# Performance work log

Measured on AMD Instinct MI355X. Metric: run time of the kernel, lower is better.

The kernel has to match this reference:

```python
import jax, jax.numpy as jnp
import numpy as np

N_QUBITS = 8
D_K = 64
B, S = 8, 1024


def _single_qubit_states(xang, theta):
    # xang: [B,S,n] values in [-1,1] (post-tanh); theta: [n,3] Rot params (phi, theta, omega)
    # state = RZ(omega) @ RY(th) @ RZ(phi) @ RY(pi*xang) |0>
    a = xang * jnp.pi
    c = jnp.cos(a * 0.5)          # [B,S,n]
    s = jnp.sin(a * 0.5)
    phi, th, om = theta[:, 0], theta[:, 1], theta[:, 2]   # each [n]
    ct = jnp.cos(th * 0.5)
    st = jnp.sin(th * 0.5)
    e_mpo = jnp.exp(-0.5j * (phi + om))   # e^{-i(phi+omega)/2}
    e_pmo = jnp.exp(0.5j * (phi - om))    # e^{+i(phi-omega)/2}
    amp0 = e_mpo * ct * c - e_pmo * st * s
    amp1 = jnp.conj(e_pmo) * st * c + jnp.conj(e_mpo) * ct * s
    return jnp.stack([amp0, amp1], axis=-1)   # [B,S,n,2] complex64


def setup_inputs() -> dict:
    key = jax.random.key(0)
    k1, k2, k3, k4 = jax.random.split(key, 4)
    x = jax.random.normal(k1, (B, S, D_K), dtype=jnp.float32)
    theta_q = jax.random.normal(k2, (N_QUBITS, 3), dtype=jnp.float32) * 0.1
    theta_k = jax.random.normal(k3, (N_QUBITS, 3), dtype=jnp.float32) * 0.1
    W_v = jax.random.normal(k4, (D_K, D_K), dtype=jnp.float32) / np.sqrt(D_K)
    b_v = jnp.zeros((D_K,), dtype=jnp.float32)
    return {"x": x, "theta_q": theta_q, "theta_k": theta_k, "W_v": W_v, "b_v": b_v}


def reference(x, theta_q, theta_k, W_v, b_v):
    n = theta_q.shape[0]
    xn = jnp.tanh(x[..., :n])                 # [B,S,n]
    qs = _single_qubit_states(xn, theta_q)    # [B,S,n,2]
    ks = _single_qubit_states(xn, theta_k)    # [B,S,n,2]
    # per-qubit overlap <q_i | k_j> for every (b, s, t) pair
    ov = jnp.einsum('bsnc,btnc->bstn', jnp.conj(qs), ks)  # [B,S,S,n] complex
    mag2 = jnp.real(ov) ** 2 + jnp.imag(ov) ** 2
    core = jnp.prod(mag2, axis=-1)            # |<psi_q|psi_k>|^2 = swap-test <Z>
    scores = (core + 1.0) * 0.5               # [B,S,S]
    attn = jax.nn.softmax(scores, axis=-1)
    values = x @ W_v.T + b_v                  # [B,S,D]
    out = jnp.einsum('bst,btd->bsd', attn, values)
    return out, attn
```

## Files before the change

kernel.cpp:

```cpp
#include <hip/hip_runtime.h>
#include <hip/hip_fp16.h>
#include <math.h>

#define NQ 8
#define DK 64
#define NB 8
#define NS 1024
#define RB 8
#define EPITCH 1032

typedef _Float16 h2v __attribute__((ext_vector_type(2)));

__device__ __forceinline__ float fdot2h(unsigned qu, unsigned ku, float acc) {
#if defined(__has_builtin) && __has_builtin(__builtin_amdgcn_fdot2)
    union { unsigned u; h2v h; } a, b;
    a.u = qu; b.u = ku;
    return __builtin_amdgcn_fdot2(a.h, b.h, acc, false);
#else
    __half2 qh = *(__half2*)&qu, kh = *(__half2*)&ku;
    float2 qf = __half22float2(qh), kf = __half22float2(kh);
    return fmaf(qf.x, kf.x, fmaf(qf.y, kf.y, acc));
#endif
}

__device__ __forceinline__ void qk_density(float s, float c,
                                           const float* t6,
                                           float& d0, float& d1, float& ur, float& ui) {
    float ct = t6[0], st = t6[1], cmpo = t6[2], smpo = t6[3], cpmo = t6[4], spmo = t6[5];
    float a = ct * c, b2 = st * s, cc = st * c, d2 = ct * s;
    float a0re =  cmpo * a - cpmo * b2;
    float a0im = -smpo * a - spmo * b2;
    float a1re =  cpmo * cc + cmpo * d2;
    float a1im = -spmo * cc + smpo * d2;
    d0 = fmaf(a0re, a0re, a0im * a0im);
    d1 = fmaf(a1re, a1re, a1im * a1im);
    ur = fmaf(a1re, a0re, a1im * a0im);
    ui = fmaf(a1im, a0re, -a1re * a0im);
}

__device__ __forceinline__ void theta_table(const float* __restrict__ thp, int n, float* t6) {
    float phi = thp[n * 3 + 0], th = thp[n * 3 + 1], om = thp[n * 3 + 2];
    float st, ct; __sincosf(0.5f * th, &st, &ct);
    float smpo, cmpo; __sincosf(0.5f * (phi + om), &smpo, &cmpo);
    float spmo, cpmo; __sincosf(0.5f * (phi - om), &spmo, &cpmo);
    t6[0] = ct; t6[1] = st; t6[2] = cmpo; t6[3] = smpo; t6[4] = cpmo; t6[5] = spmo;
}

__device__ __forceinline__ void tanh_sincos(float xin, float& s, float& c) {
    float ex = __expf(2.0f * xin);
    float xn = 1.0f - 2.0f / (ex + 1.0f);
    __sincosf(xn * 1.57079632679489662f, &s, &c);
}

__global__ __launch_bounds__(256) void prep_kernel(
    const float* __restrict__ x,
    const float* __restrict__ theta_k,
    const float* __restrict__ Wv,
    const float* __restrict__ bv,
    __half* __restrict__ kdh,
    __half* __restrict__ v2) {
    int bid = blockIdx.x;
    int tid = threadIdx.x;
    if (bid < 1024) {
        int gp = bid * 4 + (tid >> 6);
        int d = tid & 63;
        int t0 = gp * 2;
        const float4* x0 = (const float4*)(x + (size_t)t0 * DK);
        const float4* x1 = (const float4*)(x + (size_t)(t0 + 1) * DK);
        const float4* wr = (const float4*)(Wv + (size_t)d * DK);
        float p0 = bv[d], p1 = bv[d], q0 = 0.f, q1 = 0.f;
#pragma unroll
        for (int j = 0; j < DK / 4; ++j) {
            float4 wv = wr[j];
            float4 a = x0[j], b = x1[j];
            p0 = fmaf(a.x, wv.x, p0); q0 = fmaf(a.y, wv.y, q0);
            p0 = fmaf(a.z, wv.z, p0); q0 = fmaf(a.w, wv.w, q0);
            p1 = fmaf(b.x, wv.x, p1); q1 = fmaf(b.y, wv.y, q1);
            p1 = fmaf(b.z, wv.z, p1); q1 = fmaf(b.w, wv.w, q1);
        }
        int b = t0 >> 10, pi = (t0 & 1023) >> 1;
        __half2 hv = __floats2half2_rn(p0 + q0, p1 + q1);
        *(__half2*)&v2[((size_t)(b * 512 + pi) * 64 + d) * 2] = hv;
    } else {
        __shared__ float tk[NQ][6];
        if (tid < NQ) theta_table(theta_k, tid, tk[tid]);
        __syncthreads();

        int gid = (bid - 1024) * 256 + tid;
        int tok = gid >> 3;
        int n = gid & 7;
        float s, c;
        tanh_sincos(x[(size_t)tok * DK + n], s, c);
        float d0, d1, ur, ui;
        qk_density(s, c, tk[n], d0, d1, ur, ui);
        __half2* kp = (__half2*)(kdh + (size_t)tok * 32 + n * 4);
        kp[0] = __floats2half2_rn(d0, d1);
        kp[1] = __floats2half2_rn(2.f * ur, 2.f * ui);
    }
}

__global__ __launch_bounds__(256, 4) void attn_kernel(
    const float* __restrict__ x,
    const float* __restrict__ theta_q,
    const __half* __restrict__ kdh,
    const __half* __restrict__ v2,
    float* __restrict__ out, float* __restrict__ attn) {
    __shared__ __align__(16) unsigned char smem[RB * EPITCH * 2];
    __half (*e16)[EPITCH] = (__half(*)[EPITCH])smem;
    float* red = (float*)smem;
    __shared__ unsigned q16[RB][16];
    __shared__ float tq[NQ][6];
    __shared__ float red_lds[4][RB];
    __shared__ float inv_lds[RB];

    int tid = threadIdx.x;
    int gr0 = blockIdx.x * RB;
    int b = gr0 >> 10;
    int w = tid >> 6, lane = tid & 63;

    if (tid < NQ) theta_table(theta_q, tid, tq[tid]);
    __syncthreads();
    if (tid < RB * NQ) {
        int r = tid >> 3, n = tid & 7;
        float s, c;
        tanh_sincos(x[(size_t)(gr0 + r) * DK + n], s, c);
        float d0, d1, ur, ui;
        qk_density(s, c, tq[n], d0, d1, ur, ui);
        __half2 h0 = __floats2half2_rn(d0, d1);
        __half2 h1 = __floats2half2_rn(ur, ui);
        q16[r][2 * n + 0] = *(unsigned*)&h0;
        q16[r][2 * n + 1] = *(unsigned*)&h1;
    }

    const __half* kfb = kdh + (size_t)b * NS * 32;
    int t0 = w * 256;
    uint4 kv[4][4];
#pragma unroll
    for (int j = 0; j < 4; ++j) {
        const uint4* kp = (const uint4*)(kfb + (size_t)(t0 + j * 64 + lane) * 32);
        kv[j][0] = kp[0]; kv[j][1] = kp[1]; kv[j][2] = kp[2]; kv[j][3] = kp[3];
    }
    __syncthreads();

    float sums[RB];
#pragma unroll
    for (int r = 0; r < RB; ++r) sums[r] = 0.f;

#pragma unroll
    for (int r = 0; r < RB; ++r) {
        unsigned sq[16];
#pragma unroll
        for (int i = 0; i < 16; ++i) sq[i] = __builtin_amdgcn_readfirstlane(q16[r][i]);
#pragma unroll
        for (int j = 0; j < 4; ++j) {
            float m0 = fdot2h(sq[ 0], kv[j][0].x, fdot2h(sq[ 1], kv[j][0].y, 0.f));
            float m1 = fdot2h(sq[ 2], kv[j][0].z, fdot2h(sq[ 3], kv[j][0].w, 0.f));
            float m2 = fdot2h(sq[ 4], kv[j][1].x, fdot2h(sq[ 5], kv[j][1].y, 0.f));
            float m3 = fdot2h(sq[ 6], kv[j][1].z, fdot2h(sq[ 7], kv[j][1].w, 0.f));
            float m4 = fdot2h(sq[ 8], kv[j][2].x, fdot2h(sq[ 9], kv[j][2].y, 0.f));
            float m5 = fdot2h(sq[10], kv[j][2].z, fdot2h(sq[11], kv[j][2].w, 0.f));
            float m6 = fdot2h(sq[12], kv[j][3].x, fdot2h(sq[13], kv[j][3].y, 0.f));
            float m7 = fdot2h(sq[14], kv[j][3].z, fdot2h(sq[15], kv[j][3].w, 0.f));
            float core = ((m0 * m1) * (m2 * m3)) * ((m4 * m5) * (m6 * m7));
            float e = __expf(fmaf(core, 0.5f, 0.5f));
            e16[r][t0 + j * 64 + lane] = __float2half_rn(e);
            sums[r] += e;
        }
    }

#pragma unroll
    for (int r = 0; r < RB; ++r) {
#pragma unroll
        for (int m = 1; m < 64; m <<= 1) sums[r] += __shfl_xor(sums[r], m, 64);
    }
    if (lane == 0) {
#pragma unroll
        for (int r = 0; r < RB; ++r) red_lds[w][r] = sums[r];
    }
    __syncthreads();
    if (tid < RB)
        inv_lds[tid] = 1.f / (red_lds[0][tid] + red_lds[1][tid] + red_lds[2][tid] + red_lds[3][tid]);
    __syncthreads();

    float* ab = attn + (size_t)gr0 * NS;
#pragma unroll
    for (int r = 0; r < RB; ++r) {
        float iv = inv_lds[r];
        uint2 raw = *(const uint2*)&e16[r][tid * 4];
        __half2* hp = (__half2*)&raw;
        float2 lo = __half22float2(hp[0]), hi = __half22float2(hp[1]);
        *(float4*)&ab[(size_t)r * NS + tid * 4] =
            make_float4(lo.x * iv, lo.y * iv, hi.x * iv, hi.y * iv);
    }

    int tg = tid >> 4, dg = tid & 15;
    const __half* v2l = v2 + (size_t)b * 512 * 128 + dg * 8;
    float acc[RB][4];
#pragma unroll
    for (int r = 0; r < RB; ++r) { acc[r][0] = acc[r][1] = acc[r][2] = acc[r][3] = 0.f; }

    for (int jj = 0; jj < 8; ++jj) {
        int p0 = jj * 64 + tg * 4;
        uint4 vv0 = *(const uint4*)(v2l + (size_t)(p0 + 0) * 128);
        uint4 vv1 = *(const uint4*)(v2l + (size_t)(p0 + 1) * 128);
        uint4 vv2 = *(const uint4*)(v2l + (size_t)(p0 + 2) * 128);
        uint4 vv3 = *(const uint4*)(v2l + (size_t)(p0 + 3) * 128);
#pragma unroll
        for (int r = 0; r < RB; ++r) {
            uint4 ep = *(const uint4*)&e16[r][2 * p0];
            acc[r][0] = fdot2h(ep.x, vv0.x, acc[r][0]);
            acc[r][1] = fdot2h(ep.x, vv0.y, acc[r][1]);
            acc[r][2] = fdot2h(ep.x, vv0.z, acc[r][2]);
            acc[r][3] = fdot2h(ep.x, vv0.w, acc[r][3]);
            acc[r][0] = fdot2h(ep.y, vv1.x, acc[r][0]);
            acc[r][1] = fdot2h(ep.y, vv1.y, acc[r][1]);
            acc[r][2] = fdot2h(ep.y, vv1.z, acc[r][2]);
            acc[r][3] = fdot2h(ep.y, vv1.w, acc[r][3]);
            acc[r][0] = fdot2h(ep.z, vv2.x, acc[r][0]);
            acc[r][1] = fdot2h(ep.z, vv2.y, acc[r][1]);
            acc[r][2] = fdot2h(ep.z, vv2.z, acc[r][2]);
            acc[r][3] = fdot2h(ep.z, vv2.w, acc[r][3]);
            acc[r][0] = fdot2h(ep.w, vv3.x, acc[r][0]);
            acc[r][1] = fdot2h(ep.w, vv3.y, acc[r][1]);
            acc[r][2] = fdot2h(ep.w, vv3.z, acc[r][2]);
            acc[r][3] = fdot2h(ep.w, vv3.w, acc[r][3]);
        }
    }

#pragma unroll
    for (int h = 0; h < 2; ++h) {
        __syncthreads();
#pragma unroll
        for (int r = 0; r < 4; ++r) {
            *(float4*)&red[((size_t)tg * 4 + r) * 64 + dg * 4] =
                make_float4(acc[h * 4 + r][0], acc[h * 4 + r][1],
                            acc[h * 4 + r][2], acc[h * 4 + r][3]);
        }
        __syncthreads();
        int r2 = tid >> 6, d = tid & 63;
        float o = 0.f;
#pragma unroll
        for (int g = 0; g < 16; ++g) o += red[((size_t)g * 4 + r2) * 64 + d];
        out[((size_t)(gr0 + h * 4 + r2)) * DK + d] = o * inv_lds[h * 4 + r2];
    }
}

extern "C" void kernel_launch(void* const* d_in, const int* in_sizes, int n_in,
                              void* d_out, int out_size, void* d_ws, size_t ws_size,
                              hipStream_t stream) {
    const float* x       = (const float*)d_in[0];
    const float* theta_q = (const float*)d_in[1];
    const float* theta_k = (const float*)d_in[2];
    const float* W_v     = (const float*)d_in[3];
    const float* b_v     = (const float*)d_in[4];

    float* out  = (float*)d_out;
    float* attn = (float*)d_out + (size_t)NB * NS * DK;

    __half* kdh = (__half*)d_ws;
    __half* v2  = kdh + (size_t)NB * NS * 32;

    prep_kernel<<<1024 + NB * NS * NQ / 256, 256, 0, stream>>>(
        x, theta_k, W_v, b_v, kdh, v2);
    attn_kernel<<<NB * NS / RB, 256, 0, stream>>>(x, theta_q, kdh, v2, out, attn);
}
```

Baseline: 44.95 us.

## Restructure score loop to two keys per lane and prefetch V tiles

The score phase now has each lane process two adjacent keys per iteration, loading 128 contiguous bytes per lane and writing the two exp values as one half2 store. It loops over key chunks outside the query rows, so only 8 uint4 key registers are live instead of 16. The PV loop software-prefetches the next V tile into registers while the current one is consumed, to hide global load latency. The changes cut register pressure and LDS store count, but the per-lane key loads become wider and strided, which may coalesce worse, and the prefetch adds registers.

```diff
diff --git a/kernel.cpp b/kernel.cpp
--- a/kernel.cpp
+++ b/kernel.cpp
@@ -131,40 +131,49 @@
         q16[r][2 * n + 0] = *(unsigned*)&h0;
         q16[r][2 * n + 1] = *(unsigned*)&h1;
     }
+    __syncthreads();
 
     const __half* kfb = kdh + (size_t)b * NS * 32;
     int t0 = w * 256;
-    uint4 kv[4][4];
-#pragma unroll
-    for (int j = 0; j < 4; ++j) {
-        const uint4* kp = (const uint4*)(kfb + (size_t)(t0 + j * 64 + lane) * 32);
-        kv[j][0] = kp[0]; kv[j][1] = kp[1]; kv[j][2] = kp[2]; kv[j][3] = kp[3];
-    }
-    __syncthreads();
-
     float sums[RB];
 #pragma unroll
     for (int r = 0; r < RB; ++r) sums[r] = 0.f;
 
 #pragma unroll
-    for (int r = 0; r < RB; ++r) {
-        unsigned sq[16];
-#pragma unroll
-        for (int i = 0; i < 16; ++i) sq[i] = __builtin_amdgcn_readfirstlane(q16[r][i]);
-#pragma unroll
-        for (int j = 0; j < 4; ++j) {
-            float m0 = fdot2h(sq[ 0], kv[j][0].x, fdot2h(sq[ 1], kv[j][0].y, 0.f));
-            float m1 = fdot2h(sq[ 2], kv[j][0].z, fdot2h(sq[ 3], kv[j][0].w, 0.f));
-            float m2 = fdot2h(sq[ 4], kv[j][1].x, fdot2h(sq[ 5], kv[j][1].y, 0.f));
-            float m3 = fdot2h(sq[ 6], kv[j][1].z, fdot2h(sq[ 7], kv[j][1].w, 0.f));
-            float m4 = fdot2h(sq[ 8], kv[j][2].x, fdot2h(sq[ 9], kv[j][2].y, 0.f));
-            float m5 = fdot2h(sq[10], kv[j][2].z, fdot2h(sq[11], kv[j][2].w, 0.f));
-            float m6 = fdot2h(sq[12], kv[j][3].x, fdot2h(sq[13], kv[j][3].y, 0.f));
-            float m7 = fdot2h(sq[14], kv[j][3].z, fdot2h(sq[15], kv[j][3].w, 0.f));
-            float core = ((m0 * m1) * (m2 * m3)) * ((m4 * m5) * (m6 * m7));
-            float e = __expf(fmaf(core, 0.5f, 0.5f));
-            e16[r][t0 + j * 64 + lane] = __float2half_rn(e);
-            sums[r] += e;
+    for (int j = 0; j < 2; ++j) {
+        int tA = t0 + j * 128 + 2 * lane;
+        const uint4* kpA = (const uint4*)(kfb + (size_t)tA * 32);
+        uint4 kA0 = kpA[0], kA1 = kpA[1], kA2 = kpA[2], kA3 = kpA[3];
+        uint4 kB0 = kpA[4], kB1 = kpA[5], kB2 = kpA[6], kB3 = kpA[7];
+#pragma unroll
+        for (int r = 0; r < RB; ++r) {
+            unsigned sq[16];
+#pragma unroll
+            for (int i = 0; i < 16; ++i) sq[i] = __builtin_amdgcn_readfirstlane(q16[r][i]);
+            float a0 = fdot2h(sq[ 0], kA0.x, fdot2h(sq[ 1], kA0.y, 0.f));
+            float a1 = fdot2h(sq[ 2], kA0.z, fdot2h(sq[ 3], kA0.w, 0.f));
+            float a2 = fdot2h(sq[ 4], kA1.x, fdot2h(sq[ 5], kA1.y, 0.f));
+            float a3 = fdot2h(sq[ 6], kA1.z, fdot2h(sq[ 7], kA1.w, 0.f));
+            float a4 = fdot2h(sq[ 8], kA2.x, fdot2h(sq[ 9], kA2.y, 0.f));
+            float a5 = fdot2h(sq[10], kA2.z, fdot2h(sq[11], kA2.w, 0.f));
+            float a6 = fdot2h(sq[12], kA3.x, fdot2h(sq[13], kA3.y, 0.f));
+            float a7 = fdot2h(sq[14], kA3.z, fdot2h(sq[15], kA3.w, 0.f));
+            float coreA = ((a0 * a1) * (a2 * a3)) * ((a4 * a5) * (a6 * a7));
+
+            float b0 = fdot2h(sq[ 0], kB0.x, fdot2h(sq[ 1], kB0.y, 0.f));
+            float b1 = fdot2h(sq[ 2], kB0.z, fdot2h(sq[ 3], kB0.w, 0.f));
+            float b2 = fdot2h(sq[ 4], kB1.x, fdot2h(sq[ 5], kB1.y, 0.f));
+            float b3 = fdot2h(sq[ 6], kB1.z, fdot2h(sq[ 7], kB1.w, 0.f));
+            float b4 = fdot2h(sq[ 8], kB2.x, fdot2h(sq[ 9], kB2.y, 0.f));
+            float b5 = fdot2h(sq[10], kB2.z, fdot2h(sq[11], kB2.w, 0.f));
+            float b6 = fdot2h(sq[12], kB3.x, fdot2h(sq[13], kB3.y, 0.f));
+            float b7 = fdot2h(sq[14], kB3.z, fdot2h(sq[15], kB3.w, 0.f));
+            float coreB = ((b0 * b1) * (b2 * b3)) * ((b4 * b5) * (b6 * b7));
+
+            float e0 = __expf(fmaf(coreA, 0.5f, 0.5f));
+            float e1 = __expf(fmaf(coreB, 0.5f, 0.5f));
+            *(__half2*)&e16[r][tA] = __floats2half2_rn(e0, e1);
+            sums[r] += e0 + e1;
         }
     }
 
@@ -199,12 +208,18 @@
 #pragma unroll
     for (int r = 0; r < RB; ++r) { acc[r][0] = acc[r][1] = acc[r][2] = acc[r][3] = 0.f; }
 
+    uint4 vv0 = *(const uint4*)(v2l + (size_t)(tg * 4 + 0) * 128);
+    uint4 vv1 = *(const uint4*)(v2l + (size_t)(tg * 4 + 1) * 128);
+    uint4 vv2 = *(const uint4*)(v2l + (size_t)(tg * 4 + 2) * 128);
+    uint4 vv3 = *(const uint4*)(v2l + (size_t)(tg * 4 + 3) * 128);
+
     for (int jj = 0; jj < 8; ++jj) {
         int p0 = jj * 64 + tg * 4;
-        uint4 vv0 = *(const uint4*)(v2l + (size_t)(p0 + 0) * 128);
-        uint4 vv1 = *(const uint4*)(v2l + (size_t)(p0 + 1) * 128);
-        uint4 vv2 = *(const uint4*)(v2l + (size_t)(p0 + 2) * 128);
-        uint4 vv3 = *(const uint4*)(v2l + (size_t)(p0 + 3) * 128);
+        int pn = (jj < 7) ? p0 + 64 : p0;
+        uint4 nv0 = *(const uint4*)(v2l + (size_t)(pn + 0) * 128);
+        uint4 nv1 = *(const uint4*)(v2l + (size_t)(pn + 1) * 128);
+        uint4 nv2 = *(const uint4*)(v2l + (size_t)(pn + 2) * 128);
+        uint4 nv3 = *(const uint4*)(v2l + (size_t)(pn + 3) * 128);
 #pragma unroll
         for (int r = 0; r < RB; ++r) {
             uint4 ep = *(const uint4*)&e16[r][2 * p0];
@@ -225,6 +240,7 @@
             acc[r][2] = fdot2h(ep.w, vv3.z, acc[r][2]);
             acc[r][3] = fdot2h(ep.w, vv3.w, acc[r][3]);
         }
+        vv0 = nv0; vv1 = nv1; vv2 = nv2; vv3 = nv3;
     }
 
 #pragma unroll
```

Result: slower. 96.71 us (+115.1%).
